# Kernel optimization log

Hardware: AMD Instinct MI355X
Metric: run time of the kernel (lower is better)

The kernel has to match this reference:

```python
import jax, jax.numpy as jnp
import numpy as np

N_NODES = 50000
N_EDGES = 800000
D = 64  # in_dim = hidden = out_dim
LEAKY_SLOPE = 0.01  # F.leaky_relu default


def gat_layer(h, src, dst, W, b, aW, ab):
    # fc: z = h @ W.T + b            [N, D_out]
    z = h @ W.T + b
    zs = z[src]                       # gather src feats  [E, D_out]
    zd = z[dst]                       # gather dst feats  [E, D_out]
    # attn_fc(concat(z_src, z_dst)) -> scalar per edge, then leaky_relu
    e = jnp.concatenate([zs, zd], axis=-1) @ aW.T + ab   # [E, 1]
    e = jax.nn.leaky_relu(e, LEAKY_SLOPE)[:, 0]          # [E]
    # softmax over incoming edges per destination node (mailbox softmax)
    m = jax.ops.segment_max(e, dst, num_segments=N_NODES)    # [N]
    ex = jnp.exp(e - m[dst])
    den = jax.ops.segment_sum(ex, dst, num_segments=N_NODES)  # [N]
    alpha = ex / den[dst]                                      # [E]
    # scatter-sum aggregate of alpha * z_src
    return jax.ops.segment_sum(alpha[:, None] * zs, dst, num_segments=N_NODES)


def setup_inputs() -> dict:
    key = jax.random.key(0)
    ks = jax.random.split(key, 16)
    x = jax.random.normal(ks[0], (N_NODES, D), dtype=jnp.float32)
    src = jax.random.randint(ks[1], (N_EDGES,), 0, N_NODES)
    dst = jax.random.randint(ks[2], (N_EDGES,), 0, N_NODES)
    # xavier_normal with relu gain, per reset_parameters
    gain = float(np.sqrt(2.0))
    params = {}
    for i in range(3):
        std_fc = gain * np.sqrt(2.0 / (D + D))
        std_at = gain * np.sqrt(2.0 / (2 * D + 1))
        params[f"W{i}"] = jax.random.normal(ks[3 + 4 * i], (D, D), dtype=jnp.float32) * std_fc
        params[f"b{i}"] = jnp.zeros((D,), dtype=jnp.float32)
        params[f"a{i}"] = jax.random.normal(ks[4 + 4 * i], (1, 2 * D), dtype=jnp.float32) * std_at
        params[f"ab{i}"] = jnp.zeros((1,), dtype=jnp.float32)
    return {"x": x, "src": src, "dst": dst, **params}


def reference(x, src, dst, W0, b0, a0, ab0, W1, b1, a1, ab1, W2, b2, a2, ab2):
    h = gat_layer(x, src, dst, W0, b0, a0, ab0)
    h = jax.nn.relu(h)
    h = gat_layer(h, src, dst, W1, b1, a1, ab1)
    h = jax.nn.relu(h)
    h = gat_layer(h, src, dst, W2, b2, a2, ab2)
    return h
```

## Files before the change

### kernel.cpp

```cpp
#include <hip/hip_runtime.h>
#include <math.h>

#define N_NODES 50000
#define N_EDGES 800000
#define D 64

#define NB 256
#define NBLK 256
#define BUCKET_NODES 196
#define TILE 3125

typedef unsigned short ushort_t;

__device__ __forceinline__ ushort_t f32_to_bf16(float f) {
    unsigned u = __float_as_uint(f);
    u += 0x7fffu + ((u >> 16) & 1u);
    return (ushort_t)(u >> 16);
}

template<int N>
__global__ void scan_partial_g(const int* __restrict__ in, int* __restrict__ partials) {
    const int base = blockIdx.x * 1024 + threadIdx.x * 4;
    int4 c = make_int4(0, 0, 0, 0);
    if (base + 3 < N) c = *(const int4*)&in[base];
    else { int* cp = (int*)&c; for (int j = 0; j < 4; ++j) if (base + j < N) cp[j] = in[base + j]; }
    int s = c.x + c.y + c.z + c.w;
    #pragma unroll
    for (int off = 32; off >= 1; off >>= 1) s += __shfl_xor(s, off, 64);
    __shared__ int red[4];
    if ((threadIdx.x & 63) == 0) red[threadIdx.x >> 6] = s;
    __syncthreads();
    if (threadIdx.x == 0) partials[blockIdx.x] = red[0] + red[1] + red[2] + red[3];
}

__global__ void scan_offsets_g(int* __restrict__ partials, int nt, int* __restrict__ total_out) {
    const int lane = threadIdx.x;
    const int v = (lane < nt) ? partials[lane] : 0;
    int inc = v;
    #pragma unroll
    for (int off = 1; off < 64; off <<= 1) {
        const int w = __shfl_up(inc, off, 64);
        if (lane >= off) inc += w;
    }
    if (lane < nt) partials[lane] = inc - v;
    if (total_out != nullptr && lane == 63) *total_out = inc;
}

template<int N>
__global__ void scan_write_g(const int* __restrict__ in, const int* __restrict__ partials,
                             int* __restrict__ out) {
    const int tid  = threadIdx.x;
    const int base = blockIdx.x * 1024 + tid * 4;
    int4 c = make_int4(0, 0, 0, 0);
    if (base + 3 < N) c = *(const int4*)&in[base];
    else { int* cp = (int*)&c; for (int j = 0; j < 4; ++j) if (base + j < N) cp[j] = in[base + j]; }
    const int s = c.x + c.y + c.z + c.w;
    __shared__ int sh[256];
    sh[tid] = s;
    __syncthreads();
    for (int off = 1; off < 256; off <<= 1) {
        const int w = (tid >= off) ? sh[tid - off] : 0;
        __syncthreads();
        sh[tid] += w;
        __syncthreads();
    }
    int run = partials[blockIdx.x] + sh[tid] - s;
    const int* cp = (const int*)&c;
    int rp[4];
    #pragma unroll
    for (int j = 0; j < 4; ++j) { rp[j] = run; run += cp[j]; }
    if (base + 3 < N) *(int4*)&out[base] = make_int4(rp[0], rp[1], rp[2], rp[3]);
    else for (int j = 0; j < 4; ++j) if (base + j < N) out[base + j] = rp[j];
}

__global__ __launch_bounds__(256) void bucket_hist(const int* __restrict__ dst,
                                                   int* __restrict__ Acnt) {
    __shared__ int hist[NB];
    for (int i = threadIdx.x; i < NB; i += 256) hist[i] = 0;
    __syncthreads();
    const int base = blockIdx.x * TILE;
    for (int i = threadIdx.x; i < TILE; i += 256)
        atomicAdd(&hist[dst[base + i] / BUCKET_NODES], 1);
    __syncthreads();
    for (int bk = threadIdx.x; bk < NB; bk += 256)
        Acnt[bk * NBLK + blockIdx.x] = hist[bk];
}

__global__ __launch_bounds__(256) void bucket_scatter(const int* __restrict__ src,
                                                      const int* __restrict__ dst,
                                                      const int* __restrict__ offs,
                                                      int2* __restrict__ staging) {
    __shared__ int cur[NB];
    for (int i = threadIdx.x; i < NB; i += 256) cur[i] = offs[i * NBLK + blockIdx.x];
    __syncthreads();
    const int base = blockIdx.x * TILE;
    for (int i = threadIdx.x; i < TILE; i += 256) {
        const int s = src[base + i], d = dst[base + i];
        const int pos = atomicAdd(&cur[d / BUCKET_NODES], 1);
        staging[pos] = make_int2(s, d);
    }
}

__global__ __launch_bounds__(256) void node_counts(const int2* __restrict__ staging,
                                                   const int* __restrict__ offs,
                                                   int* __restrict__ counts) {
    __shared__ int cnt[BUCKET_NODES];
    const int b = blockIdx.x;
    for (int i = threadIdx.x; i < BUCKET_NODES; i += 256) cnt[i] = 0;
    __syncthreads();
    const int s0 = offs[b * NBLK];
    const int s1 = (b == NB - 1) ? N_EDGES : offs[(b + 1) * NBLK];
    for (int i = s0 + threadIdx.x; i < s1; i += 256)
        atomicAdd(&cnt[staging[i].y - b * BUCKET_NODES], 1);
    __syncthreads();
    for (int i = threadIdx.x; i < BUCKET_NODES; i += 256) {
        const int node = b * BUCKET_NODES + i;
        if (node < N_NODES) counts[node] = cnt[i];
    }
}

__global__ __launch_bounds__(256) void bucket_to_csr(const int2* __restrict__ staging,
                                                     const int* __restrict__ offs,
                                                     const int* __restrict__ row_ptr,
                                                     int* __restrict__ csr_src) {
    __shared__ int cur[BUCKET_NODES];
    const int b = blockIdx.x;
    for (int i = threadIdx.x; i < BUCKET_NODES; i += 256) {
        const int node = b * BUCKET_NODES + i;
        cur[i] = (node < N_NODES) ? row_ptr[node] : 0;
    }
    __syncthreads();
    const int s0 = offs[b * NBLK];
    const int s1 = (b == NB - 1) ? N_EDGES : offs[(b + 1) * NBLK];
    for (int i = s0 + threadIdx.x; i < s1; i += 256) {
        const int2 e = staging[i];
        const int pos = atomicAdd(&cur[e.y - b * BUCKET_NODES], 1);
        csr_src[pos] = e.x;
    }
}

__global__ void hist_kernel(const int* __restrict__ dst, int* __restrict__ counts) {
    const int i = blockIdx.x * blockDim.x + threadIdx.x;
    if (i < N_EDGES) atomicAdd(&counts[dst[i]], 1);
}
__global__ void copy_kernel(const int* __restrict__ in, int* __restrict__ out, int n) {
    const int i = blockIdx.x * blockDim.x + threadIdx.x;
    if (i < n) out[i] = in[i];
}
__global__ void scatter_kernel(const int* __restrict__ src, const int* __restrict__ dst,
                               int* __restrict__ cursor, int* __restrict__ csr_src) {
    const int i = blockIdx.x * blockDim.x + threadIdx.x;
    if (i >= N_EDGES) return;
    const int pos = atomicAdd(&cursor[dst[i]], 1);
    csr_src[pos] = src[i];
}

#define NL_ROWS 8
__global__ __launch_bounds__(256) void node_linear_gemm(
    const float* __restrict__ h, ushort_t* __restrict__ zb,
    const float* __restrict__ W, const float* __restrict__ b,
    const float* __restrict__ a, const float* __restrict__ ab,
    float* __restrict__ s_src, float* __restrict__ s_dst)
{
    __shared__ float Wt[64 * 65];
    for (int idx = threadIdx.x; idx < D * D; idx += 256) {
        const int j = idx >> 6, k = idx & 63;
        Wt[k * 65 + j] = W[idx];
    }
    __syncthreads();

    const int lane = threadIdx.x & 63;
    const int wv   = __builtin_amdgcn_readfirstlane(threadIdx.x >> 6);
    const int row0 = (blockIdx.x * 4 + wv) * NL_ROWS;
    if (row0 >= N_NODES) return;

    const float bj  = b[lane];
    const float alo = a[lane];
    const float ahi = a[64 + lane];

    const float* hr[NL_ROWS];
    #pragma unroll
    for (int r = 0; r < NL_ROWS; ++r) hr[r] = h + (size_t)(row0 + r) * D;

    float acc[NL_ROWS];
    #pragma unroll
    for (int r = 0; r < NL_ROWS; ++r) acc[r] = bj;

    #pragma unroll 4
    for (int k = 0; k < D; ++k) {
        const float wkj = Wt[k * 65 + lane];
        #pragma unroll
        for (int r = 0; r < NL_ROWS; ++r)
            acc[r] = fmaf(hr[r][k], wkj, acc[r]);
    }

    #pragma unroll
    for (int r = 0; r < NL_ROWS; ++r) {
        zb[(size_t)(row0 + r) * D + lane] = f32_to_bf16(acc[r]);
        float u = acc[r] * alo;
        float v = acc[r] * ahi;
        #pragma unroll
        for (int off = 32; off >= 1; off >>= 1) {
            u += __shfl_xor(u, off, 64);
            v += __shfl_xor(v, off, 64);
        }
        if (lane == 0) { s_src[row0 + r] = u; s_dst[row0 + r] = v + ab[0]; }
    }
}

__global__ __launch_bounds__(256) void edge_softmax(
    const int* __restrict__ row_ptr, const int* __restrict__ csr_src,
    const float* __restrict__ s_src, const float* __restrict__ s_dst,
    float* __restrict__ raw, int2* __restrict__ wgtsi)
{
    const int lane = threadIdx.x & 63;
    const int sl   = lane & 15;
    const int g    = lane >> 4;
    const int wid  = blockIdx.x * 4 + (threadIdx.x >> 6);
    const int node = wid * 4 + g;
    if (node >= N_NODES) return;
    const int beg = row_ptr[node];
    const int end = row_ptr[node + 1];
    if (beg == end) return;
    const float sd = s_dst[node];

    float m = -INFINITY, den = 0.f;
    for (int base = beg; base < end; base += 16) {
        const int n = min(16, end - base);
        float e = -INFINITY;
        if (sl < n) {
            const int s = csr_src[base + sl];
            e = s_src[s] + sd;
            e = e > 0.f ? e : 0.01f * e;
            raw[base + sl] = e;
        }
        float mc = e;
        #pragma unroll
        for (int off = 8; off >= 1; off >>= 1) mc = fmaxf(mc, __shfl_xor(mc, off, 64));
        if (mc > m) { den *= __expf(m - mc); m = mc; }
        float ex = (sl < n) ? __expf(e - m) : 0.f;
        #pragma unroll
        for (int off = 8; off >= 1; off >>= 1) ex += __shfl_xor(ex, off, 64);
        den += ex;
    }
    const float inv = 1.f / den;
    for (int base = beg; base < end; base += 16) {
        const int n = min(16, end - base);
        if (sl < n) {
            const int i = base + sl;
            const float w = __expf(raw[i] - m) * inv;
            wgtsi[i] = make_int2(__float_as_int(w), csr_src[i]);
        }
    }
}

template<bool RELU>
__global__ __launch_bounds__(256) void weighted_gather(
    const int* __restrict__ row_ptr, const int2* __restrict__ wgtsi,
    const ushort_t* __restrict__ zb, float* __restrict__ out)
{
    __shared__ int2 sh[4][64];
    const int lane = threadIdx.x & 63;
    const int wv   = threadIdx.x >> 6;
    const int node = blockIdx.x * 4 + wv;
    if (node >= N_NODES) return;
    const int beg = row_ptr[node];
    const int end = row_ptr[node + 1];
    const int half = lane >> 5;
    const int fl   = lane & 31;

    float2 acc[8];
    #pragma unroll
    for (int p = 0; p < 8; ++p) acc[p] = make_float2(0.f, 0.f);

    for (int base = beg; base < end; base += 64) {
        const int n = min(64, end - base);
        sh[wv][lane] = (lane < n) ? wgtsi[base + lane] : make_int2(0, 0);
        for (int t = 0; t < n; t += 16) {
            #pragma unroll
            for (int p = 0; p < 8; ++p) {
                const int ei = t + 2 * p + half;
                const int2 ws = sh[wv][ei];
                const float w = __int_as_float(ws.x);
                const unsigned u = *(const unsigned*)&zb[(size_t)ws.y * D + 2 * fl];
                acc[p].x = fmaf(w, __uint_as_float(u << 16), acc[p].x);
                acc[p].y = fmaf(w, __uint_as_float(u & 0xffff0000u), acc[p].y);
            }
        }
    }
    float2 tot = make_float2(0.f, 0.f);
    #pragma unroll
    for (int p = 0; p < 8; ++p) { tot.x += acc[p].x; tot.y += acc[p].y; }
    tot.x += __shfl_xor(tot.x, 32, 64);
    tot.y += __shfl_xor(tot.y, 32, 64);
    if (RELU) { tot.x = fmaxf(tot.x, 0.f); tot.y = fmaxf(tot.y, 0.f); }
    if (half == 0)
        *(float2*)&out[(size_t)node * D + 2 * fl] = tot;
}

extern "C" void kernel_launch(void* const* d_in, const int* in_sizes, int n_in,
                              void* d_out, int out_size, void* d_ws, size_t ws_size,
                              hipStream_t stream) {
    const float* x   = (const float*)d_in[0];
    const int*   src = (const int*)d_in[1];
    const int*   dst = (const int*)d_in[2];
    float* out = (float*)d_out;

    char* wp = (char*)d_ws;
    auto alloc = [&](size_t bytes) -> void* {
        void* p = (void*)wp;
        wp += (bytes + 255) & ~(size_t)255;
        return p;
    };
    ushort_t* zb   = (ushort_t*)alloc((size_t)N_NODES * D * sizeof(ushort_t));
    float* s_src   = (float*)alloc((size_t)N_NODES * sizeof(float));
    float* s_dst   = (float*)alloc((size_t)N_NODES * sizeof(float));
    int*   counts  = (int*)alloc((size_t)N_NODES * sizeof(int));
    int*   row_ptr = (int*)alloc((size_t)(N_NODES + 1) * sizeof(int));
    int*   csr_src = (int*)alloc((size_t)N_EDGES * sizeof(int));
    int*   partA   = (int*)alloc(64 * sizeof(int));
    int*   partB   = (int*)alloc(64 * sizeof(int));
    float* raw     = (float*)alloc((size_t)N_EDGES * sizeof(float));
    int2*  wgtsi   = (int2*)alloc((size_t)N_EDGES * sizeof(int2));
    int*   cursor  = (int*)alloc((size_t)N_NODES * sizeof(int));
    int*   Acnt    = (int*)alloc((size_t)NB * NBLK * sizeof(int));
    int*   offs    = (int*)alloc((size_t)NB * NBLK * sizeof(int));
    int2*  staging = (int2*)alloc((size_t)N_EDGES * sizeof(int2));
    size_t bucket_used = (size_t)(wp - (char*)d_ws);

    const bool use_bucket = (ws_size >= bucket_used);

    if (use_bucket) {
        bucket_hist<<<NBLK, 256, 0, stream>>>(dst, Acnt);
        scan_partial_g<NB * NBLK><<<64, 256, 0, stream>>>(Acnt, partB);
        scan_offsets_g<<<1, 64, 0, stream>>>(partB, 64, nullptr);
        scan_write_g<NB * NBLK><<<64, 256, 0, stream>>>(Acnt, partB, offs);
        bucket_scatter<<<NBLK, 256, 0, stream>>>(src, dst, offs, staging);
        node_counts<<<NB, 256, 0, stream>>>(staging, offs, counts);
        scan_partial_g<N_NODES><<<49, 256, 0, stream>>>(counts, partA);
        scan_offsets_g<<<1, 64, 0, stream>>>(partA, 49, &row_ptr[N_NODES]);
        scan_write_g<N_NODES><<<49, 256, 0, stream>>>(counts, partA, row_ptr);
        bucket_to_csr<<<NB, 256, 0, stream>>>(staging, offs, row_ptr, csr_src);
    } else {
        hipMemsetAsync(counts, 0, (size_t)N_NODES * sizeof(int), stream);
        hist_kernel<<<(N_EDGES + 255) / 256, 256, 0, stream>>>(dst, counts);
        scan_partial_g<N_NODES><<<49, 256, 0, stream>>>(counts, partA);
        scan_offsets_g<<<1, 64, 0, stream>>>(partA, 49, &row_ptr[N_NODES]);
        scan_write_g<N_NODES><<<49, 256, 0, stream>>>(counts, partA, row_ptr);
        copy_kernel<<<(N_NODES + 255) / 256, 256, 0, stream>>>(row_ptr, cursor, N_NODES);
        scatter_kernel<<<(N_EDGES + 255) / 256, 256, 0, stream>>>(src, dst, cursor, csr_src);
    }

    const int grid_k1  = (N_NODES + 4 * NL_ROWS - 1) / (4 * NL_ROWS);
    const int grid_sm  = (N_NODES + 15) / 16;
    const int grid_agg = (N_NODES + 3) / 4;

    for (int layer = 0; layer < 3; ++layer) {
        const float* W  = (const float*)d_in[3 + 4 * layer];
        const float* b  = (const float*)d_in[4 + 4 * layer];
        const float* a  = (const float*)d_in[5 + 4 * layer];
        const float* ab = (const float*)d_in[6 + 4 * layer];
        const float* hin = (layer == 0) ? x : out;

        node_linear_gemm<<<grid_k1, 256, 0, stream>>>(hin, zb, W, b, a, ab, s_src, s_dst);
        edge_softmax<<<grid_sm, 256, 0, stream>>>(row_ptr, csr_src, s_src, s_dst, raw, wgtsi);
        if (layer < 2) {
            weighted_gather<true ><<<grid_agg, 256, 0, stream>>>(row_ptr, wgtsi, zb, out);
        } else {
            weighted_gather<false><<<grid_agg, 256, 0, stream>>>(row_ptr, wgtsi, zb, out);
        }
    }
}
```

Baseline: 210.8 us.

## Fuse edge softmax into weighted gather and shorten CSR build launch chain

Merges the edge softmax and weighted gather kernels into one per-layer kernel. Each wave computes max and denominator for four nodes, then recomputes edge weights on the fly while gathering, so the raw and packed weight buffers are no longer written and read back. The CSR build also drops launches: the partial-offset scan is folded into the write kernel, and row_ptr comes from per-bucket sums in a single kernel. The fallback non-bucket path is removed. In exchange, csr_src and s_src are read twice and the exp is recomputed for every edge.

Measured after the change: 199.6 us. 5.3% less time.

```diff
diff --git a/kernel.cpp b/kernel.cpp
--- a/kernel.cpp
+++ b/kernel.cpp
@@ -33,29 +33,27 @@
     if (threadIdx.x == 0) partials[blockIdx.x] = red[0] + red[1] + red[2] + red[3];
 }
 
-__global__ void scan_offsets_g(int* __restrict__ partials, int nt, int* __restrict__ total_out) {
-    const int lane = threadIdx.x;
-    const int v = (lane < nt) ? partials[lane] : 0;
-    int inc = v;
-    #pragma unroll
-    for (int off = 1; off < 64; off <<= 1) {
-        const int w = __shfl_up(inc, off, 64);
-        if (lane >= off) inc += w;
-    }
-    if (lane < nt) partials[lane] = inc - v;
-    if (total_out != nullptr && lane == 63) *total_out = inc;
-}
-
-template<int N>
-__global__ void scan_write_g(const int* __restrict__ in, const int* __restrict__ partials,
+template<int N, int NT>
+__global__ void scan_write_i(const int* __restrict__ in, const int* __restrict__ partials_raw,
                              int* __restrict__ out) {
-    const int tid  = threadIdx.x;
+    __shared__ int toff;
+    __shared__ int sh[256];
+    const int tid = threadIdx.x;
+    if (tid < 64) {
+        const int v = (tid < NT) ? partials_raw[tid] : 0;
+        int inc = v;
+        #pragma unroll
+        for (int off = 1; off < 64; off <<= 1) {
+            const int w = __shfl_up(inc, off, 64);
+            if (tid >= off) inc += w;
+        }
+        if (tid == blockIdx.x) toff = inc - v;
+    }
     const int base = blockIdx.x * 1024 + tid * 4;
     int4 c = make_int4(0, 0, 0, 0);
     if (base + 3 < N) c = *(const int4*)&in[base];
     else { int* cp = (int*)&c; for (int j = 0; j < 4; ++j) if (base + j < N) cp[j] = in[base + j]; }
     const int s = c.x + c.y + c.z + c.w;
-    __shared__ int sh[256];
     sh[tid] = s;
     __syncthreads();
     for (int off = 1; off < 256; off <<= 1) {
@@ -64,7 +62,7 @@
         sh[tid] += w;
         __syncthreads();
     }
-    int run = partials[blockIdx.x] + sh[tid] - s;
+    int run = toff + sh[tid] - s;
     const int* cp = (const int*)&c;
     int rp[4];
     #pragma unroll
@@ -103,20 +101,57 @@
 
 __global__ __launch_bounds__(256) void node_counts(const int2* __restrict__ staging,
                                                    const int* __restrict__ offs,
-                                                   int* __restrict__ counts) {
+                                                   int* __restrict__ counts,
+                                                   int* __restrict__ bucket_sum) {
     __shared__ int cnt[BUCKET_NODES];
-    const int b = blockIdx.x;
-    for (int i = threadIdx.x; i < BUCKET_NODES; i += 256) cnt[i] = 0;
+    __shared__ int red[4];
+    const int b = blockIdx.x, tid = threadIdx.x;
+    for (int i = tid; i < BUCKET_NODES; i += 256) cnt[i] = 0;
     __syncthreads();
     const int s0 = offs[b * NBLK];
     const int s1 = (b == NB - 1) ? N_EDGES : offs[(b + 1) * NBLK];
-    for (int i = s0 + threadIdx.x; i < s1; i += 256)
+    for (int i = s0 + tid; i < s1; i += 256)
         atomicAdd(&cnt[staging[i].y - b * BUCKET_NODES], 1);
     __syncthreads();
-    for (int i = threadIdx.x; i < BUCKET_NODES; i += 256) {
+    for (int i = tid; i < BUCKET_NODES; i += 256) {
         const int node = b * BUCKET_NODES + i;
         if (node < N_NODES) counts[node] = cnt[i];
     }
+    int s = (tid < BUCKET_NODES) ? cnt[tid] : 0;
+    #pragma unroll
+    for (int off = 32; off >= 1; off >>= 1) s += __shfl_xor(s, off, 64);
+    if ((tid & 63) == 0) red[tid >> 6] = s;
+    __syncthreads();
+    if (tid == 0) bucket_sum[b] = red[0] + red[1] + red[2] + red[3];
+}
+
+__global__ __launch_bounds__(256) void row_ptr_build(const int* __restrict__ counts,
+                                                     const int* __restrict__ bucket_sum,
+                                                     int* __restrict__ row_ptr) {
+    __shared__ int bs[NB];
+    __shared__ int loc[256];
+    const int b = blockIdx.x, tid = threadIdx.x;
+    bs[tid] = bucket_sum[tid];
+    __syncthreads();
+    for (int off = 1; off < 256; off <<= 1) {
+        const int w = (tid >= off) ? bs[tid - off] : 0;
+        __syncthreads();
+        bs[tid] += w;
+        __syncthreads();
+    }
+    const int bucket_off = bs[b] - bucket_sum[b];
+    const int node = b * BUCKET_NODES + tid;
+    const int c = (tid < BUCKET_NODES && node < N_NODES) ? counts[node] : 0;
+    loc[tid] = c;
+    __syncthreads();
+    for (int off = 1; off < 256; off <<= 1) {
+        const int w = (tid >= off) ? loc[tid - off] : 0;
+        __syncthreads();
+        loc[tid] += w;
+        __syncthreads();
+    }
+    if (tid < BUCKET_NODES && node < N_NODES) row_ptr[node] = bucket_off + loc[tid] - c;
+    if (b == 0 && tid == 0) row_ptr[N_NODES] = N_EDGES;
 }
 
 __global__ __launch_bounds__(256) void bucket_to_csr(const int2* __restrict__ staging,
@@ -137,22 +172,6 @@
         const int pos = atomicAdd(&cur[e.y - b * BUCKET_NODES], 1);
         csr_src[pos] = e.x;
     }
-}
-
-__global__ void hist_kernel(const int* __restrict__ dst, int* __restrict__ counts) {
-    const int i = blockIdx.x * blockDim.x + threadIdx.x;
-    if (i < N_EDGES) atomicAdd(&counts[dst[i]], 1);
-}
-__global__ void copy_kernel(const int* __restrict__ in, int* __restrict__ out, int n) {
-    const int i = blockIdx.x * blockDim.x + threadIdx.x;
-    if (i < n) out[i] = in[i];
-}
-__global__ void scatter_kernel(const int* __restrict__ src, const int* __restrict__ dst,
-                               int* __restrict__ cursor, int* __restrict__ csr_src) {
-    const int i = blockIdx.x * blockDim.x + threadIdx.x;
-    if (i >= N_EDGES) return;
-    const int pos = atomicAdd(&cursor[dst[i]], 1);
-    csr_src[pos] = src[i];
 }
 
 #define NL_ROWS 8
@@ -208,22 +227,24 @@
     }
 }
 
-__global__ __launch_bounds__(256) void edge_softmax(
+template<bool RELU>
+__global__ __launch_bounds__(256) void fused_softmax_gather(
     const int* __restrict__ row_ptr, const int* __restrict__ csr_src,
     const float* __restrict__ s_src, const float* __restrict__ s_dst,
-    float* __restrict__ raw, int2* __restrict__ wgtsi)
+    const ushort_t* __restrict__ zb, float* __restrict__ out)
 {
+    __shared__ int2 sh[4][64];
     const int lane = threadIdx.x & 63;
+    const int wv   = threadIdx.x >> 6;
+    const int g    = lane >> 4;
     const int sl   = lane & 15;
-    const int g    = lane >> 4;
-    const int wid  = blockIdx.x * 4 + (threadIdx.x >> 6);
-    const int node = wid * 4 + g;
-    if (node >= N_NODES) return;
-    const int beg = row_ptr[node];
-    const int end = row_ptr[node + 1];
-    if (beg == end) return;
-    const float sd = s_dst[node];
-
+    const int node0 = (blockIdx.x * 4 + wv) * 4;
+    if (node0 >= N_NODES) return;
+    const int mynode = node0 + g;
+
+    const int beg = row_ptr[mynode];
+    const int end = row_ptr[mynode + 1];
+    const float sd = s_dst[mynode];
     float m = -INFINITY, den = 0.f;
     for (int base = beg; base < end; base += 16) {
         const int n = min(16, end - base);
@@ -232,7 +253,6 @@
             const int s = csr_src[base + sl];
             e = s_src[s] + sd;
             e = e > 0.f ? e : 0.01f * e;
-            raw[base + sl] = e;
         }
         float mc = e;
         #pragma unroll
@@ -243,59 +263,54 @@
         for (int off = 8; off >= 1; off >>= 1) ex += __shfl_xor(ex, off, 64);
         den += ex;
     }
-    const float inv = 1.f / den;
-    for (int base = beg; base < end; base += 16) {
-        const int n = min(16, end - base);
-        if (sl < n) {
-            const int i = base + sl;
-            const float w = __expf(raw[i] - m) * inv;
-            wgtsi[i] = make_int2(__float_as_int(w), csr_src[i]);
-        }
-    }
-}
-
-template<bool RELU>
-__global__ __launch_bounds__(256) void weighted_gather(
-    const int* __restrict__ row_ptr, const int2* __restrict__ wgtsi,
-    const ushort_t* __restrict__ zb, float* __restrict__ out)
-{
-    __shared__ int2 sh[4][64];
-    const int lane = threadIdx.x & 63;
-    const int wv   = threadIdx.x >> 6;
-    const int node = blockIdx.x * 4 + wv;
-    if (node >= N_NODES) return;
-    const int beg = row_ptr[node];
-    const int end = row_ptr[node + 1];
+    const float invden = (den > 0.f) ? 1.f / den : 0.f;
+
     const int half = lane >> 5;
     const int fl   = lane & 31;
-
-    float2 acc[8];
-    #pragma unroll
-    for (int p = 0; p < 8; ++p) acc[p] = make_float2(0.f, 0.f);
-
-    for (int base = beg; base < end; base += 64) {
-        const int n = min(64, end - base);
-        sh[wv][lane] = (lane < n) ? wgtsi[base + lane] : make_int2(0, 0);
-        for (int t = 0; t < n; t += 16) {
-            #pragma unroll
-            for (int p = 0; p < 8; ++p) {
-                const int ei = t + 2 * p + half;
-                const int2 ws = sh[wv][ei];
-                const float w = __int_as_float(ws.x);
-                const unsigned u = *(const unsigned*)&zb[(size_t)ws.y * D + 2 * fl];
-                acc[p].x = fmaf(w, __uint_as_float(u << 16), acc[p].x);
-                acc[p].y = fmaf(w, __uint_as_float(u & 0xffff0000u), acc[p].y);
+    #pragma unroll
+    for (int q = 0; q < 4; ++q) {
+        const int nq    = node0 + q;
+        const int begq  = __shfl(beg, q * 16, 64);
+        const int endq  = __shfl(end, q * 16, 64);
+        const float mq  = __shfl(m, q * 16, 64);
+        const float ivq = __shfl(invden, q * 16, 64);
+        const float sdq = __shfl(sd, q * 16, 64);
+
+        float2 acc[8];
+        #pragma unroll
+        for (int p = 0; p < 8; ++p) acc[p] = make_float2(0.f, 0.f);
+
+        for (int base = begq; base < endq; base += 64) {
+            const int n = min(64, endq - base);
+            int2 ws = make_int2(0, 0);
+            if (lane < n) {
+                const int s = csr_src[base + lane];
+                float e = s_src[s] + sdq;
+                e = e > 0.f ? e : 0.01f * e;
+                ws = make_int2(__float_as_int(__expf(e - mq) * ivq), s);
             }
-        }
-    }
-    float2 tot = make_float2(0.f, 0.f);
-    #pragma unroll
-    for (int p = 0; p < 8; ++p) { tot.x += acc[p].x; tot.y += acc[p].y; }
-    tot.x += __shfl_xor(tot.x, 32, 64);
-    tot.y += __shfl_xor(tot.y, 32, 64);
-    if (RELU) { tot.x = fmaxf(tot.x, 0.f); tot.y = fmaxf(tot.y, 0.f); }
-    if (half == 0)
-        *(float2*)&out[(size_t)node * D + 2 * fl] = tot;
+            sh[wv][lane] = ws;
+            for (int t = 0; t < n; t += 16) {
+                #pragma unroll
+                for (int p = 0; p < 8; ++p) {
+                    const int ei = t + 2 * p + half;
+                    const int2 w2 = sh[wv][ei];
+                    const float w = __int_as_float(w2.x);
+                    const unsigned u = *(const unsigned*)&zb[(size_t)w2.y * D + 2 * fl];
+                    acc[p].x = fmaf(w, __uint_as_float(u << 16), acc[p].x);
+                    acc[p].y = fmaf(w, __uint_as_float(u & 0xffff0000u), acc[p].y);
+                }
+            }
+        }
+        float2 tot = make_float2(0.f, 0.f);
+        #pragma unroll
+        for (int p = 0; p < 8; ++p) { tot.x += acc[p].x; tot.y += acc[p].y; }
+        tot.x += __shfl_xor(tot.x, 32, 64);
+        tot.y += __shfl_xor(tot.y, 32, 64);
+        if (RELU) { tot.x = fmaxf(tot.x, 0.f); tot.y = fmaxf(tot.y, 0.f); }
+        if (half == 0)
+            *(float2*)&out[(size_t)nq * D + 2 * fl] = tot;
+    }
 }
 
 extern "C" void kernel_launch(void* const* d_in, const int* in_sizes, int n_in,
@@ -312,48 +327,29 @@
         wp += (bytes + 255) & ~(size_t)255;
         return p;
     };
-    ushort_t* zb   = (ushort_t*)alloc((size_t)N_NODES * D * sizeof(ushort_t));
-    float* s_src   = (float*)alloc((size_t)N_NODES * sizeof(float));
-    float* s_dst   = (float*)alloc((size_t)N_NODES * sizeof(float));
-    int*   counts  = (int*)alloc((size_t)N_NODES * sizeof(int));
-    int*   row_ptr = (int*)alloc((size_t)(N_NODES + 1) * sizeof(int));
-    int*   csr_src = (int*)alloc((size_t)N_EDGES * sizeof(int));
-    int*   partA   = (int*)alloc(64 * sizeof(int));
-    int*   partB   = (int*)alloc(64 * sizeof(int));
-    float* raw     = (float*)alloc((size_t)N_EDGES * sizeof(float));
-    int2*  wgtsi   = (int2*)alloc((size_t)N_EDGES * sizeof(int2));
-    int*   cursor  = (int*)alloc((size_t)N_NODES * sizeof(int));
-    int*   Acnt    = (int*)alloc((size_t)NB * NBLK * sizeof(int));
-    int*   offs    = (int*)alloc((size_t)NB * NBLK * sizeof(int));
-    int2*  staging = (int2*)alloc((size_t)N_EDGES * sizeof(int2));
-    size_t bucket_used = (size_t)(wp - (char*)d_ws);
-
-    const bool use_bucket = (ws_size >= bucket_used);
-
-    if (use_bucket) {
-        bucket_hist<<<NBLK, 256, 0, stream>>>(dst, Acnt);
-        scan_partial_g<NB * NBLK><<<64, 256, 0, stream>>>(Acnt, partB);
-        scan_offsets_g<<<1, 64, 0, stream>>>(partB, 64, nullptr);
-        scan_write_g<NB * NBLK><<<64, 256, 0, stream>>>(Acnt, partB, offs);
-        bucket_scatter<<<NBLK, 256, 0, stream>>>(src, dst, offs, staging);
-        node_counts<<<NB, 256, 0, stream>>>(staging, offs, counts);
-        scan_partial_g<N_NODES><<<49, 256, 0, stream>>>(counts, partA);
-        scan_offsets_g<<<1, 64, 0, stream>>>(partA, 49, &row_ptr[N_NODES]);
-        scan_write_g<N_NODES><<<49, 256, 0, stream>>>(counts, partA, row_ptr);
-        bucket_to_csr<<<NB, 256, 0, stream>>>(staging, offs, row_ptr, csr_src);
-    } else {
-        hipMemsetAsync(counts, 0, (size_t)N_NODES * sizeof(int), stream);
-        hist_kernel<<<(N_EDGES + 255) / 256, 256, 0, stream>>>(dst, counts);
-        scan_partial_g<N_NODES><<<49, 256, 0, stream>>>(counts, partA);
-        scan_offsets_g<<<1, 64, 0, stream>>>(partA, 49, &row_ptr[N_NODES]);
-        scan_write_g<N_NODES><<<49, 256, 0, stream>>>(counts, partA, row_ptr);
-        copy_kernel<<<(N_NODES + 255) / 256, 256, 0, stream>>>(row_ptr, cursor, N_NODES);
-        scatter_kernel<<<(N_EDGES + 255) / 256, 256, 0, stream>>>(src, dst, cursor, csr_src);
-    }
-
-    const int grid_k1  = (N_NODES + 4 * NL_ROWS - 1) / (4 * NL_ROWS);
-    const int grid_sm  = (N_NODES + 15) / 16;
-    const int grid_agg = (N_NODES + 3) / 4;
+    ushort_t* zb      = (ushort_t*)alloc((size_t)N_NODES * D * sizeof(ushort_t));
+    float* s_src      = (float*)alloc((size_t)N_NODES * sizeof(float));
+    float* s_dst      = (float*)alloc((size_t)N_NODES * sizeof(float));
+    int*   counts     = (int*)alloc((size_t)N_NODES * sizeof(int));
+    int*   row_ptr    = (int*)alloc((size_t)(N_NODES + 1) * sizeof(int));
+    int*   csr_src    = (int*)alloc((size_t)N_EDGES * sizeof(int));
+    int*   partB      = (int*)alloc(64 * sizeof(int));
+    int*   bucket_sum = (int*)alloc((size_t)NB * sizeof(int));
+    int*   Acnt       = (int*)alloc((size_t)NB * NBLK * sizeof(int));
+    int*   offs       = (int*)alloc((size_t)NB * NBLK * sizeof(int));
+    int2*  staging    = (int2*)alloc((size_t)N_EDGES * sizeof(int2));
+    (void)ws_size;
+
+    bucket_hist<<<NBLK, 256, 0, stream>>>(dst, Acnt);
+    scan_partial_g<NB * NBLK><<<64, 256, 0, stream>>>(Acnt, partB);
+    scan_write_i<NB * NBLK, 64><<<64, 256, 0, stream>>>(Acnt, partB, offs);
+    bucket_scatter<<<NBLK, 256, 0, stream>>>(src, dst, offs, staging);
+    node_counts<<<NB, 256, 0, stream>>>(staging, offs, counts, bucket_sum);
+    row_ptr_build<<<NB, 256, 0, stream>>>(counts, bucket_sum, row_ptr);
+    bucket_to_csr<<<NB, 256, 0, stream>>>(staging, offs, row_ptr, csr_src);
+
+    const int grid_k1 = (N_NODES + 4 * NL_ROWS - 1) / (4 * NL_ROWS);
+    const int grid_fg = N_NODES / 16;
 
     for (int layer = 0; layer < 3; ++layer) {
         const float* W  = (const float*)d_in[3 + 4 * layer];
@@ -363,11 +359,10 @@
         const float* hin = (layer == 0) ? x : out;
 
         node_linear_gemm<<<grid_k1, 256, 0, stream>>>(hin, zb, W, b, a, ab, s_src, s_dst);
-        edge_softmax<<<grid_sm, 256, 0, stream>>>(row_ptr, csr_src, s_src, s_dst, raw, wgtsi);
         if (layer < 2) {
-            weighted_gather<true ><<<grid_agg, 256, 0, stream>>>(row_ptr, wgtsi, zb, out);
+            fused_softmax_gather<true ><<<grid_fg, 256, 0, stream>>>(row_ptr, csr_src, s_src, s_dst, zb, out);
         } else {
-            weighted_gather<false><<<grid_agg, 256, 0, stream>>>(row_ptr, wgtsi, zb, out);
-        }
-    }
-}
+            fused_softmax_gather<false><<<grid_fg, 256, 0, stream>>>(row_ptr, csr_src, s_src, s_dst, zb, out);
+        }
+    }
+}
```
